# Performance work log

Hardware: AMD Instinct MI355X
Metric: run time of the kernel (lower is better)

## Reference

```python
import jax, jax.numpy as jnp
import numpy as np

B, N, M, C = 4, 4096, 300, 1152
SA_H, SA_D = 36, 32           # linear self-attention heads / head dim
CA_H = 16                     # cross-attention heads
INNER_SA = SA_H * SA_D        # 1152
INNER_FF = int(C * 2.5)       # 2880
EPS = 1e-6


def _ln(x):
    # LayerNorm without affine, eps=1e-6
    mu = x.mean(-1, keepdims=True)
    var = x.var(-1, keepdims=True)
    return (x - mu) / jnp.sqrt(var + EPS)


def setup_inputs() -> dict:
    key = jax.random.key(0)
    ks = jax.random.split(key, 24)
    p = lambda i, shape: jax.random.normal(ks[i], shape, jnp.float32) * 0.02
    return {
        "x": jax.random.normal(ks[0], (B, N, C), jnp.float32),
        "conditioning": jax.random.normal(ks[1], (B, M, C), jnp.float32),
        "t_emb": jax.random.normal(ks[2], (B, C), jnp.float32),
        # linear self-attention (qkv has no bias)
        "w_qkv": p(3, (C, 3 * INNER_SA)),
        "w_sa_out": p(4, (INNER_SA, C)),
        "b_sa_out": jnp.zeros((C,), jnp.float32),
        # norm_cross (affine LayerNorm)
        "gamma_cross": jnp.ones((C,), jnp.float32),
        "beta_cross": jnp.zeros((C,), jnp.float32),
        # cross-attention
        "w_q": p(5, (C, C)), "b_q": jnp.zeros((C,), jnp.float32),
        "w_kv": p(6, (C, 2 * C)), "b_kv": jnp.zeros((2 * C,), jnp.float32),
        "w_co": p(7, (C, C)), "b_co": jnp.zeros((C,), jnp.float32),
        # MixFFN
        "w_fc1": p(8, (C, 2 * INNER_FF)), "b_fc1": jnp.zeros((2 * INNER_FF,), jnp.float32),
        "dw_kernel": p(9, (3, 3, 1, INNER_FF)),  # depthwise conv, HWIO
        "dw_bias": jnp.zeros((INNER_FF,), jnp.float32),
        "w_fc2": p(10, (INNER_FF, C)), "b_fc2": jnp.zeros((C,), jnp.float32),
        # adaLN modulation
        "w_ada": p(11, (C, 6 * C)), "b_ada": jnp.zeros((6 * C,), jnp.float32),
        "sst": jax.random.normal(ks[12], (6, C), jnp.float32) * 0.02,
    }


def reference(x, conditioning, t_emb, w_qkv, w_sa_out, b_sa_out,
              gamma_cross, beta_cross, w_q, b_q, w_kv, b_kv, w_co, b_co,
              w_fc1, b_fc1, dw_kernel, dw_bias, w_fc2, b_fc2,
              w_ada, b_ada, sst):
    Bx, Nx, Cx = x.shape
    ada = jax.nn.silu(t_emb) @ w_ada + b_ada          # (B, 6C)
    ada = sst[None] + ada.reshape(Bx, 6, Cx)          # (B, 6, C)
    shift_sa, scale_sa, gate_sa, shift_ff, scale_ff, gate_ff = (
        ada[:, 0], ada[:, 1], ada[:, 2], ada[:, 3], ada[:, 4], ada[:, 5])

    # --- modulated linear self-attention (ReLU kernel) ---
    xn = _ln(x) * (1.0 + scale_sa[:, None]) + shift_sa[:, None]
    qkv = (xn @ w_qkv).reshape(Bx, Nx, 3, SA_H, SA_D)
    q = jax.nn.relu(qkv[:, :, 0])
    k = jax.nn.relu(qkv[:, :, 1])
    v = qkv[:, :, 2]
    kv = jnp.einsum('bnhd,bnhe->bhde', k, v)                  # (B,H,D,D)
    out = jnp.einsum('bnhd,bhde->bnhe', q, kv)                # (B,N,H,D)
    denom = jnp.einsum('bnhd,bhd->bnh', q, k.sum(1)) + 1e-6   # (B,N,H)
    out = (out / denom[..., None]).reshape(Bx, Nx, INNER_SA)
    x = x + gate_sa[:, None] * (out @ w_sa_out + b_sa_out)

    # --- cross-attention (softmax) ---
    xc = _ln(x) * gamma_cross + beta_cross
    hd = Cx // CA_H
    qc = (xc @ w_q + b_q).reshape(Bx, Nx, CA_H, hd)
    kvc = (conditioning @ w_kv + b_kv).reshape(Bx, M, 2, CA_H, hd)
    kc, vc = kvc[:, :, 0], kvc[:, :, 1]
    attn = jnp.einsum('bnhd,bmhd->bhnm', qc, kc) * (hd ** -0.5)
    attn = jax.nn.softmax(attn, axis=-1)
    oc = jnp.einsum('bhnm,bmhd->bnhd', attn, vc).reshape(Bx, Nx, Cx)
    x = x + oc @ w_co + b_co

    # --- modulated GLU-dwconv FFN ---
    xn = _ln(x) * (1.0 + scale_ff[:, None]) + shift_ff[:, None]
    gv = xn @ w_fc1 + b_fc1
    gate, val = gv[..., :INNER_FF], gv[..., INNER_FF:]
    h = jax.nn.silu(gate) * val
    hw = int(round(Nx ** 0.5))
    h = h.reshape(Bx, hw, hw, INNER_FF)                       # NHWC
    h = jax.lax.conv_general_dilated(
        h, dw_kernel, window_strides=(1, 1), padding='SAME',
        dimension_numbers=('NHWC', 'HWIO', 'NHWC'),
        feature_group_count=INNER_FF) + dw_bias
    h = h.reshape(Bx, Nx, INNER_FF)
    x = x + gate_ff[:, None] * (h @ w_fc2 + b_fc2)
    return x
```

## Files before the change

### kernel.cpp

```cpp
#include <hip/hip_runtime.h>

typedef __bf16 bf16_t;
typedef __attribute__((ext_vector_type(8))) __bf16 bf16x8;
typedef __attribute__((ext_vector_type(4))) __bf16 bf16x4;
typedef __attribute__((ext_vector_type(4))) float f32x4;

#define DEVINL __device__ __forceinline__

DEVINL void gload16(const void* g, void* l) {
  __builtin_amdgcn_global_load_lds(
      (const __attribute__((address_space(1))) void*)g,
      (__attribute__((address_space(3))) void*)l, 16, 0, 0);
}

template <int OUT>
__global__ __launch_bounds__(512) void gemm256r(
    const bf16_t* __restrict__ A, const bf16_t* __restrict__ Bt,
    void* __restrict__ Cv, int M, int N, int K,
    const float* __restrict__ bias, const float* __restrict__ resid,
    const float* __restrict__ gate, int GM)
{
  __shared__ __align__(16) bf16_t sL[2][2][256 * 32];
  const int tid = threadIdx.x;
  const int lane = tid & 63;
  const int wave = tid >> 6;
  const int wr = wave >> 2;
  const int wc = wave & 3;

  const int nbx = gridDim.x, nby = gridDim.y;
  const int nwg = nbx * nby;
  int lin = (int)blockIdx.y * nbx + (int)blockIdx.x;
  {
    const int q = nwg >> 3, rr = nwg & 7;
    const int xcd = lin & 7, idx = lin >> 3;
    lin = (xcd < rr ? xcd * (q + 1) : rr * (q + 1) + (xcd - rr) * q) + idx;
  }
  const int per_grp = GM * nbx;
  const int gid = lin / per_grp;
  const int rem = lin - gid * per_grp;
  const int gsz = min(GM, nby - gid * GM);
  const long tileM = (long)(gid * GM + rem % gsz) * 256;
  const long tileN = (long)(rem / gsz) * 256;

  const int r0 = tid >> 2;
  const int c0 = (((tid & 3) - (r0 >> 2)) & 3) * 8;

  auto STAGE = [&](int slot, int kt) {
    const bf16_t* ga = A + (tileM + r0) * (long)K + kt + c0;
    const bf16_t* gb = Bt + (tileN + r0) * (long)K + kt + c0;
    char* la = (char*)&sL[slot][0][0] + tid * 16;
    char* lb = (char*)&sL[slot][1][0] + tid * 16;
    gload16(ga, la);
    gload16(ga + 128 * (long)K, la + 8192);
    gload16(gb, lb);
    gload16(gb + 128 * (long)K, lb + 8192);
  };

  f32x4 acc[8][4] = {};
  const int NT = K >> 5;

  STAGE(0, 0); STAGE(1, 32);
  asm volatile("s_waitcnt vmcnt(4)" ::: "memory");
  asm volatile("s_barrier" ::: "memory");

  const int r = lane & 15;
  const int kg = lane >> 4;
  const int sw = ((kg + (r >> 2)) & 3) * 16;
  const int abyte = (wr * 128 + r) * 64 + sw;
  const int bbyte = (wc * 64 + r) * 64 + sw;

  for (int t = 0; t < NT; ++t) {
    const char* pA = (const char*)&sL[t & 1][0][0];
    const char* pB = (const char*)&sL[t & 1][1][0];
    bf16x8 a[8], b[4];
#pragma unroll
    for (int n = 0; n < 4; ++n) b[n] = *(const bf16x8*)(pB + bbyte + n * 1024);
#pragma unroll
    for (int m = 0; m < 8; ++m) a[m] = *(const bf16x8*)(pA + abyte + m * 1024);
    __builtin_amdgcn_s_setprio(1);
#pragma unroll
    for (int m = 0; m < 8; ++m)
#pragma unroll
      for (int n = 0; n < 4; ++n)
        acc[m][n] = __builtin_amdgcn_mfma_f32_16x16x32_bf16(a[m], b[n],
                                                            acc[m][n], 0, 0, 0);
    __builtin_amdgcn_s_setprio(0);
    if (t + 1 >= NT) break;
    asm volatile("s_waitcnt vmcnt(0)" ::: "memory");
    asm volatile("s_barrier" ::: "memory");
    if (t + 2 < NT) STAGE(t & 1, (t + 2) << 5);
  }

  const long row0 = tileM + wr * 128 + ((lane >> 4) * 4);
  const int col0 = (int)tileN + wc * 64 + r;
#pragma unroll
  for (int m = 0; m < 8; ++m) {
#pragma unroll
    for (int n = 0; n < 4; ++n) {
      const int col = col0 + n * 16;
      if (col < N) {
        const float bb = bias ? bias[col] : 0.0f;
#pragma unroll
        for (int j = 0; j < 4; ++j) {
          const long row = row0 + m * 16 + j;
          const long idx = row * (long)N + col;
          const float v = acc[m][n][j] + bb;
          if constexpr (OUT == 1) {
            const float g = gate ? gate[(row >> 12) * 6912 + col] : 1.0f;
            const float rv = resid ? resid[idx] : 0.0f;
            ((float*)Cv)[idx] = rv + g * v;
          } else {
            ((bf16_t*)Cv)[idx] = (bf16_t)v;
          }
        }
      }
    }
  }
}

template <int OUT>
__global__ __launch_bounds__(256) void gemm_bt(
    const bf16_t* __restrict__ A, const bf16_t* __restrict__ Bt,
    void* __restrict__ Cv, int M, int N, int K,
    long strideA, long strideB, long strideC,
    const float* __restrict__ bias, const float* __restrict__ resid,
    const float* __restrict__ gate, int GM)
{
  __shared__ __align__(16) bf16_t sA[128 * 32];
  __shared__ __align__(16) bf16_t sB[128 * 32];
  const int tid = threadIdx.x;
  const int lane = tid & 63;
  const int wave = tid >> 6;
  const bf16_t* Ab = A + (size_t)blockIdx.z * strideA;
  const bf16_t* Bb = Bt + (size_t)blockIdx.z * strideB;

  const int nbx = gridDim.x, nby = gridDim.y;
  const int nwg = nbx * nby;
  int lin = (int)blockIdx.y * nbx + (int)blockIdx.x;
  {
    const int q = nwg >> 3, rr = nwg & 7;
    const int xcd = lin & 7, idx = lin >> 3;
    lin = (xcd < rr ? xcd * (q + 1) : rr * (q + 1) + (xcd - rr) * q) + idx;
  }
  const int per_grp = GM * nbx;
  const int gid = lin / per_grp;
  const int rem = lin - gid * per_grp;
  const int gsz = min(GM, nby - gid * GM);
  const long tileM = (long)(gid * GM + rem % gsz) * 128;
  const long tileN = (long)(rem / gsz) * 128;
  const int wr = wave >> 1, wc = wave & 1;

  f32x4 acc[4][4] = {};

  const int srow = lane >> 2;
  const int skcol = (lane & 3) * 8;
  const bf16_t* gA0 = Ab + (tileM + wave * 16 + srow) * (long)K + skcol;
  const bf16_t* gB0 = Bb + (tileN + wave * 16 + srow) * (long)K + skcol;
  bf16_t* lA0 = sA + wave * 512;
  bf16_t* lB0 = sB + wave * 512;
  const long rs64 = 64L * K;

  const int aoff = (wr * 64 + (lane & 15)) * 32 + (lane >> 4) * 8;
  const int boff = (wc * 64 + (lane & 15)) * 32 + (lane >> 4) * 8;

  for (int kt = 0; kt < K; kt += 32) {
    __syncthreads();
    gload16(gA0 + kt, lA0);
    gload16(gA0 + kt + rs64, lA0 + 2048);
    gload16(gB0 + kt, lB0);
    gload16(gB0 + kt + rs64, lB0 + 2048);
    __syncthreads();
    bf16x8 av[4], bv[4];
#pragma unroll
    for (int m = 0; m < 4; ++m) av[m] = *(const bf16x8*)&sA[aoff + m * 512];
#pragma unroll
    for (int n = 0; n < 4; ++n) bv[n] = *(const bf16x8*)&sB[boff + n * 512];
#pragma unroll
    for (int m = 0; m < 4; ++m)
#pragma unroll
      for (int n = 0; n < 4; ++n)
        acc[m][n] = __builtin_amdgcn_mfma_f32_16x16x32_bf16(av[m], bv[n],
                                                            acc[m][n], 0, 0, 0);
  }

  const long row0 = tileM + wr * 64 + ((lane >> 4) * 4);
  const int col0 = (int)tileN + wc * 64 + (lane & 15);
#pragma unroll
  for (int m = 0; m < 4; ++m) {
#pragma unroll
    for (int n = 0; n < 4; ++n) {
      const int col = col0 + n * 16;
      const float bb = (OUT != 2 && bias) ? bias[col] : 0.0f;
#pragma unroll
      for (int j = 0; j < 4; ++j) {
        const long row = row0 + m * 16 + j;
        const float v = acc[m][n][j] + bb;
        if constexpr (OUT == 1) {
          const long idx = row * (long)N + col;
          const float g = gate ? gate[(row >> 12) * 6912 + col] : 1.0f;
          const float rv = resid ? resid[idx] : 0.0f;
          ((float*)Cv)[idx] = rv + g * v;
        } else if constexpr (OUT == 2) {
          if (col < 72)
            ((bf16_t*)Cv)[(((long)(blockIdx.z >> 4)) * 4096 + row) * 1152 +
                          (long)(blockIdx.z & 15) * 72 + col] = (bf16_t)v;
        } else if constexpr (OUT == 3) {
          const int h = col / 72, d = col - h * 72;
          const long b = row >> 12, n4 = row & 4095;
          ((bf16_t*)Cv)[((b * 16 + h) * 4096 + n4) * 96 + d] =
              (bf16_t)(v * 0.11785113019775793f);
        } else {
          const long idx = row * (long)N + col;
          (((bf16_t*)Cv) + (size_t)blockIdx.z * strideC)[idx] = (bf16_t)v;
        }
      }
    }
  }
}

__global__ __launch_bounds__(256) void transpose_cast(
    const float* __restrict__ W, bf16_t* __restrict__ WT, int K, int N)
{
  __shared__ float tile[32][33];
  const int n0 = blockIdx.x * 32, k0 = blockIdx.y * 32;
  const int tx = threadIdx.x & 31, ty = threadIdx.x >> 5;
#pragma unroll
  for (int r = ty; r < 32; r += 8) tile[r][tx] = W[(size_t)(k0 + r) * N + n0 + tx];
  __syncthreads();
#pragma unroll
  for (int r = ty; r < 32; r += 8)
    WT[(size_t)(n0 + r) * K + k0 + tx] = (bf16_t)tile[tx][r];
}

__global__ __launch_bounds__(256) void ada_kernel(
    const float* __restrict__ t_emb, const float* __restrict__ w_ada,
    const float* __restrict__ b_ada, const float* __restrict__ sst,
    float* __restrict__ ada)
{
  __shared__ float st[4][1152];
  const int t = threadIdx.x;
  const int j = blockIdx.x * 256 + t;
  for (int i = t; i < 4 * 1152; i += 256) {
    const int b = i / 1152, cc = i % 1152;
    const float v = t_emb[b * 1152 + cc];
    st[b][cc] = v / (1.0f + __expf(-v));
  }
  __syncthreads();
  const int k0 = blockIdx.y * 144;
  float a0 = 0.f, a1 = 0.f, a2 = 0.f, a3 = 0.f;
  for (int k = k0; k < k0 + 144; ++k) {
    const float w = w_ada[(size_t)k * 6912 + j];
    a0 += st[0][k] * w; a1 += st[1][k] * w;
    a2 += st[2][k] * w; a3 += st[3][k] * w;
  }
  if (blockIdx.y == 0) {
    const float base = b_ada[j] + sst[j];
    a0 += base; a1 += base; a2 += base; a3 += base;
  }
  atomicAdd(&ada[0 * 6912 + j], a0);
  atomicAdd(&ada[1 * 6912 + j], a1);
  atomicAdd(&ada[2 * 6912 + j], a2);
  atomicAdd(&ada[3 * 6912 + j], a3);
}

__global__ __launch_bounds__(256) void ln_mod(
    const float* __restrict__ X, bf16_t* __restrict__ out,
    const float* __restrict__ adaB, int shiftIdx, int scaleIdx,
    const float* __restrict__ gamma, const float* __restrict__ beta)
{
  const int row = blockIdx.x;
  const float4* xr4 = (const float4*)(X + (size_t)row * 1152);
  float s = 0.f, s2 = 0.f;
  for (int i = threadIdx.x; i < 288; i += 256) {
    const float4 v = xr4[i];
    s += v.x + v.y + v.z + v.w;
    s2 += v.x * v.x + v.y * v.y + v.z * v.z + v.w * v.w;
  }
  const int lane = threadIdx.x & 63, wave = threadIdx.x >> 6;
#pragma unroll
  for (int o = 32; o; o >>= 1) { s += __shfl_down(s, o); s2 += __shfl_down(s2, o); }
  __shared__ float rs[4], rq[4];
  if (lane == 0) { rs[wave] = s; rq[wave] = s2; }
  __syncthreads();
  if (threadIdx.x == 0) {
    rs[0] = rs[0] + rs[1] + rs[2] + rs[3];
    rq[0] = rq[0] + rq[1] + rq[2] + rq[3];
  }
  __syncthreads();
  const float mu = rs[0] * (1.0f / 1152.0f);
  const float var = rq[0] * (1.0f / 1152.0f) - mu * mu;
  const float inv = rsqrtf(var + 1e-6f);
  const int b = row >> 12;
  const float4* shiftv = (const float4*)(adaB ? adaB + b * 6912 + shiftIdx * 1152 : beta);
  const float4* scalev = (const float4*)(adaB ? adaB + b * 6912 + scaleIdx * 1152 : gamma);
  const float add1 = adaB ? 1.0f : 0.0f;
  for (int i = threadIdx.x; i < 288; i += 256) {
    const float4 v = xr4[i];
    const float4 sc = scalev[i];
    const float4 sh = shiftv[i];
    bf16x4 o;
    o[0] = (bf16_t)((v.x - mu) * inv * (add1 + sc.x) + sh.x);
    o[1] = (bf16_t)((v.y - mu) * inv * (add1 + sc.y) + sh.y);
    o[2] = (bf16_t)((v.z - mu) * inv * (add1 + sc.z) + sh.z);
    o[3] = (bf16_t)((v.w - mu) * inv * (add1 + sc.w) + sh.w);
    *(bf16x4*)&out[(size_t)row * 1152 + i * 4] = o;
  }
}

__global__ void pad_cond_k(const float* __restrict__ cond, bf16_t* __restrict__ condp)
{
  const int idx = blockIdx.x * 256 + threadIdx.x;
  const int row = idx / 1152;
  condp[idx] = (row < 1200) ? (bf16_t)cond[idx] : (bf16_t)0.0f;
}

__global__ __launch_bounds__(256) void sa_kv_k(
    const bf16_t* __restrict__ qkv, float* __restrict__ kvb, float* __restrict__ ksumb)
{
  const int bh = blockIdx.x, b = bh / 36, h = bh % 36;
  __shared__ bf16_t sk[32][32], sv[32][32];
  const int t = threadIdx.x;
  const int nn = t >> 5, c = t & 31;
  const int srow = (t & 127) >> 2;
  const int sq4 = (t & 3) * 8;
  const int isV = t >> 7;
  float a0 = 0.f, a1 = 0.f, a2 = 0.f, a3 = 0.f, ks = 0.f;
  const size_t rowbase = (size_t)b * 4096 + (size_t)blockIdx.y * 256;
  const size_t colbase = 1152 + (size_t)isV * 1152 + h * 32 + sq4;
  for (int n0 = 0; n0 < 256; n0 += 32) {
    __syncthreads();
    const bf16x8 v8 = *(const bf16x8*)&qkv[(rowbase + n0 + srow) * 3456 + colbase];
    if (isV == 0) {
      bf16x8 r8;
#pragma unroll
      for (int j = 0; j < 8; ++j) r8[j] = (bf16_t)fmaxf((float)v8[j], 0.0f);
      *(bf16x8*)&sk[srow][sq4] = r8;
    } else {
      *(bf16x8*)&sv[srow][sq4] = v8;
    }
    __syncthreads();
#pragma unroll
    for (int q = 0; q < 32; ++q) {
      const float vv = (float)sv[q][c];
      a0 += (float)sk[q][nn] * vv;
      a1 += (float)sk[q][nn + 8] * vv;
      a2 += (float)sk[q][nn + 16] * vv;
      a3 += (float)sk[q][nn + 24] * vv;
    }
    if (t < 32) {
#pragma unroll
      for (int q = 0; q < 32; ++q) ks += (float)sk[q][t];
    }
  }
  float* kvp = kvb + (size_t)bh * 1024;
  atomicAdd(&kvp[(nn + 0) * 32 + c], a0);
  atomicAdd(&kvp[(nn + 8) * 32 + c], a1);
  atomicAdd(&kvp[(nn + 16) * 32 + c], a2);
  atomicAdd(&kvp[(nn + 24) * 32 + c], a3);
  if (t < 32) atomicAdd(&ksumb[bh * 32 + t], ks);
}

__global__ __launch_bounds__(256) void sa_out_k(
    const bf16_t* __restrict__ qkv, const float* __restrict__ kvb,
    const float* __restrict__ ksumb, bf16_t* __restrict__ so)
{
  const int row0 = blockIdx.x * 8;
  const int b = row0 >> 12;
  __shared__ float q[8][1152];
  __shared__ float denom[8][36];
  const int t = threadIdx.x;
  for (int i = t; i < 1152; i += 256) {
    const int r = i / 144, c0 = (i % 144) * 8;
    const bf16x8 v8 = *(const bf16x8*)&qkv[(size_t)(row0 + r) * 3456 + c0];
#pragma unroll
    for (int j = 0; j < 8; ++j) q[r][c0 + j] = fmaxf((float)v8[j], 0.0f);
  }
  __syncthreads();
  for (int i = t; i < 288; i += 256) {
    int r = i / 36, h = i % 36;
    const float* ksp = ksumb + (b * 36 + h) * 32;
    float dsum = 1e-6f;
#pragma unroll
    for (int d = 0; d < 32; ++d) dsum += q[r][h * 32 + d] * ksp[d];
    denom[r][h] = dsum;
  }
  __syncthreads();
  for (int j = t; j < 1152; j += 256) {
    const int h = j >> 5, e = j & 31;
    const float* kvp = kvb + ((size_t)(b * 36 + h)) * 1024 + e;
    float kreg[32];
#pragma unroll
    for (int d = 0; d < 32; ++d) kreg[d] = kvp[d * 32];
#pragma unroll
    for (int r = 0; r < 8; ++r) {
      float a = 0.f;
#pragma unroll
      for (int d = 0; d < 32; ++d) a += q[r][h * 32 + d] * kreg[d];
      so[(size_t)(row0 + r) * 1152 + j] = (bf16_t)(a / denom[r][h]);
    }
  }
}

__global__ void ca_qrepack(const bf16_t* __restrict__ qc, bf16_t* __restrict__ qcp, int b)
{
  const size_t idx = (size_t)blockIdx.x * 256 + threadIdx.x;
  const int d = (int)(idx % 96);
  const size_t r = idx / 96;
  const int n = (int)(r & 4095);
  const int h = (int)(r >> 12);
  float v = 0.f;
  if (d < 72) v = (float)qc[((size_t)(b * 4096 + n)) * 1152 + h * 72 + d] * 0.11785113019775793f;
  qcp[idx] = (bf16_t)v;
}

__global__ void ca_kcrepack(const bf16_t* __restrict__ kvc, bf16_t* __restrict__ kcp, int b)
{
  const size_t idx = (size_t)blockIdx.x * 256 + threadIdx.x;
  const int d = (int)(idx % 96);
  const size_t r = idx / 96;
  const int m = (int)(r % 384);
  const int h = (int)(r / 384);
  bf16_t v = (bf16_t)0.0f;
  if (d < 72 && m < 300) v = kvc[((size_t)(b * 300 + m)) * 2304 + h * 72 + d];
  kcp[idx] = v;
}

__global__ void ca_vtrepack(const bf16_t* __restrict__ kvc, bf16_t* __restrict__ vt, int b)
{
  const size_t idx = (size_t)blockIdx.x * 256 + threadIdx.x;
  const int m = (int)(idx % 384);
  const size_t r = idx / 384;
  const int d = (int)(r & 127);
  const int h = (int)(r >> 7);
  bf16_t v = (bf16_t)0.0f;
  if (d < 72 && m < 300) v = kvc[((size_t)(b * 300 + m)) * 2304 + 1152 + h * 72 + d];
  vt[idx] = v;
}

__global__ __launch_bounds__(256) void softmax_k(bf16_t* __restrict__ s)
{
  const int row = blockIdx.x * 4 + (threadIdx.x >> 6);
  const int lane = threadIdx.x & 63;
  bf16_t* sr = s + (size_t)row * 384;
  float v[5];
  float mx = -1e30f;
#pragma unroll
  for (int i = 0; i < 5; ++i) {
    const int m = lane + 64 * i;
    v[i] = (m < 300) ? (float)sr[m] : -1e30f;
    mx = fmaxf(mx, v[i]);
  }
#pragma unroll
  for (int o = 32; o; o >>= 1) mx = fmaxf(mx, __shfl_xor(mx, o));
  float sum = 0.f;
#pragma unroll
  for (int i = 0; i < 5; ++i) { v[i] = __expf(v[i] - mx); sum += v[i]; }
#pragma unroll
  for (int o = 32; o; o >>= 1) sum += __shfl_xor(sum, o);
  const float inv = 1.0f / sum;
#pragma unroll
  for (int i = 0; i < 5; ++i) {
    const int m = lane + 64 * i;
    if (m < 320) sr[m] = (bf16_t)(v[i] * inv);
  }
}

__global__ void glu_k(const bf16_t* __restrict__ gv, bf16_t* __restrict__ h)
{
  const size_t idx = (size_t)blockIdx.x * 256 + threadIdx.x;
  const size_t row = idx / 360;
  const int c0 = (int)(idx % 360) * 8;
  const bf16x8 g8 = *(const bf16x8*)&gv[row * 5760 + c0];
  const bf16x8 v8 = *(const bf16x8*)&gv[row * 5760 + 2880 + c0];
  bf16x8 o;
#pragma unroll
  for (int j = 0; j < 8; ++j) {
    const float g = (float)g8[j];
    const float sg = g / (1.0f + __expf(-g));
    o[j] = (bf16_t)(sg * (float)v8[j]);
  }
  *(bf16x8*)&h[row * 2880 + c0] = o;
}

__global__ __launch_bounds__(256) void dwconv_k(
    const bf16_t* __restrict__ h, const float* __restrict__ wk,
    const float* __restrict__ wb, bf16_t* __restrict__ hc)
{
  const size_t idx = (size_t)blockIdx.x * 256 + threadIdx.x;
  const int c8 = (int)(idx % 360);
  size_t p = idx / 360;
  const int x = (int)(p & 63);
  const int y = (int)(p >> 6);
  const int c0 = c8 * 8;
  float acc[8];
#pragma unroll
  for (int j = 0; j < 8; ++j) acc[j] = wb[c0 + j];
  for (int ky = -1; ky <= 1; ++ky) {
    const int yy = y + ky;
    if (yy < 0 || yy > 63) continue;
    for (int kx = -1; kx <= 1; ++kx) {
      const int xx = x + kx;
      if (xx < 0 || xx > 63) continue;
      const bf16x8 v = *(const bf16x8*)&h[((size_t)(yy * 64 + xx)) * 2880 + c0];
      const float* w = wk + ((ky + 1) * 3 + (kx + 1)) * 2880 + c0;
#pragma unroll
      for (int j = 0; j < 8; ++j) acc[j] += (float)v[j] * w[j];
    }
  }
  bf16x8 o;
#pragma unroll
  for (int j = 0; j < 8; ++j) o[j] = (bf16_t)acc[j];
  *(bf16x8*)&hc[((size_t)(y * 64 + x)) * 2880 + c0] = o;
}

extern "C" void kernel_launch(void* const* d_in, const int* in_sizes, int n_in,
                              void* d_out, int out_size, void* d_ws, size_t ws_size,
                              hipStream_t stream)
{
  const float* x          = (const float*)d_in[0];
  const float* cond       = (const float*)d_in[1];
  const float* t_emb      = (const float*)d_in[2];
  const float* w_qkv      = (const float*)d_in[3];
  const float* w_sa_out   = (const float*)d_in[4];
  const float* b_sa_out   = (const float*)d_in[5];
  const float* gamma_cr   = (const float*)d_in[6];
  const float* beta_cr    = (const float*)d_in[7];
  const float* w_q        = (const float*)d_in[8];
  const float* b_q        = (const float*)d_in[9];
  const float* w_kv       = (const float*)d_in[10];
  const float* b_kv       = (const float*)d_in[11];
  const float* w_co       = (const float*)d_in[12];
  const float* b_co       = (const float*)d_in[13];
  const float* w_fc1      = (const float*)d_in[14];
  const float* b_fc1      = (const float*)d_in[15];
  const float* dw_kernel  = (const float*)d_in[16];
  const float* dw_bias    = (const float*)d_in[17];
  const float* w_fc2      = (const float*)d_in[18];
  const float* b_fc2      = (const float*)d_in[19];
  const float* w_ada      = (const float*)d_in[20];
  const float* b_ada      = (const float*)d_in[21];
  const float* sst        = (const float*)d_in[22];
  float* out = (float*)d_out;

  char* ws = (char*)d_ws;
  size_t off = 0;
  auto alloc = [&](size_t bytes) -> char* {
    off = (off + 255) & ~(size_t)255;
    char* p = ws + off;
    off += bytes;
    return p;
  };

  bf16_t* wqkvT  = (bf16_t*)alloc((size_t)3584 * 1152 * 2);
  bf16_t* wsaT   = (bf16_t*)alloc((size_t)1280 * 1152 * 2);
  bf16_t* wqT    = (bf16_t*)alloc((size_t)1280 * 1152 * 2);
  bf16_t* wkvT   = (bf16_t*)alloc((size_t)2304 * 1152 * 2);
  bf16_t* wcoT   = (bf16_t*)alloc((size_t)1280 * 1152 * 2);
  bf16_t* wfc1T  = (bf16_t*)alloc((size_t)5888 * 1152 * 2);
  bf16_t* wfc2T  = (bf16_t*)alloc((size_t)1280 * 2880 * 2);
  float*  adaB   = (float*)alloc((size_t)4 * 6912 * 4);
  bf16_t* xn     = (bf16_t*)alloc((size_t)16384 * 1152 * 2);
  bf16_t* buf37  = (bf16_t*)alloc((size_t)16384 * 1152 * 2);
  float*  kvb    = (float*)alloc((size_t)144 * 1024 * 4);
  float*  ksumb  = (float*)alloc((size_t)144 * 32 * 4);
  bf16_t* condp  = (bf16_t*)alloc((size_t)1280 * 1152 * 2);
  bf16_t* kvcB   = (bf16_t*)alloc((size_t)1280 * 2304 * 2);

  const size_t ARENA_SMALL = (size_t)16384 * 3456 * 2;
  const size_t CA_Q = (size_t)64 * 4096 * 96 * 2;
  const size_t CA_K = (size_t)64 * 384 * 96 * 2;
  const size_t CA_V = (size_t)64 * 128 * 384 * 2;
  const size_t CA_S = (size_t)64 * 4096 * 384 * 2;
  const size_t ARENA_BIG = CA_Q + CA_K + CA_V + CA_S;
  const bool big = (off + 512 + ARENA_BIG) <= ws_size;
  char* arena = alloc(big ? ARENA_BIG : ARENA_SMALL);
  if (off > ws_size) return;

  bf16_t* qkvB = (bf16_t*)arena;
  bf16_t *qcp, *kcp, *vcT, *scores;
  if (big) {
    qcp    = (bf16_t*)arena;
    kcp    = (bf16_t*)(arena + CA_Q);
    vcT    = (bf16_t*)(arena + CA_Q + CA_K);
    scores = (bf16_t*)(arena + CA_Q + CA_K + CA_V);
  } else {
    qcp    = (bf16_t*)arena;
    kcp    = (bf16_t*)(arena + 12582912);
    vcT    = (bf16_t*)(arena + 12582912 + 1179648);
    scores = (bf16_t*)(arena + 12582912 + 1179648 + 1572864);
  }
  bf16_t *gvB, *hB, *hcB;
  if (big) {
    gvB = (bf16_t*)arena;
    hB  = (bf16_t*)(arena + (size_t)8192 * 5760 * 2);
    hcB = (bf16_t*)(arena + (size_t)8192 * 5760 * 2 + (size_t)8192 * 2880 * 2);
  } else {
    hcB = (bf16_t*)arena;
    gvB = (bf16_t*)(arena + (size_t)8192 * 2880 * 2);
    hB  = buf37;
  }

  hipMemsetAsync(adaB, 0, (size_t)4 * 6912 * 4, stream);
  hipMemsetAsync(kvb, 0, (size_t)144 * 1024 * 4, stream);
  hipMemsetAsync(ksumb, 0, (size_t)144 * 32 * 4, stream);

  transpose_cast<<<dim3(108, 36), 256, 0, stream>>>(w_qkv, wqkvT, 1152, 3456);
  transpose_cast<<<dim3(36, 36), 256, 0, stream>>>(w_sa_out, wsaT, 1152, 1152);
  transpose_cast<<<dim3(36, 36), 256, 0, stream>>>(w_q, wqT, 1152, 1152);
  transpose_cast<<<dim3(72, 36), 256, 0, stream>>>(w_kv, wkvT, 1152, 2304);
  transpose_cast<<<dim3(36, 36), 256, 0, stream>>>(w_co, wcoT, 1152, 1152);
  transpose_cast<<<dim3(180, 36), 256, 0, stream>>>(w_fc1, wfc1T, 1152, 5760);
  transpose_cast<<<dim3(36, 90), 256, 0, stream>>>(w_fc2, wfc2T, 2880, 1152);
  ada_kernel<<<dim3(27, 8), 256, 0, stream>>>(t_emb, w_ada, b_ada, sst, adaB);
  pad_cond_k<<<5760, 256, 0, stream>>>(cond, condp);

  ln_mod<<<16384, 256, 0, stream>>>(x, xn, adaB, 0, 1, nullptr, nullptr);
  gemm256r<0><<<dim3(14, 64), 512, 0, stream>>>(xn, wqkvT, qkvB, 16384, 3456, 1152,
                                                nullptr, nullptr, nullptr, 8);
  sa_kv_k<<<dim3(144, 16), 256, 0, stream>>>(qkvB, kvb, ksumb);
  sa_out_k<<<2048, 256, 0, stream>>>(qkvB, kvb, ksumb, buf37);
  gemm_bt<1><<<dim3(9, 128), 256, 0, stream>>>(buf37, wsaT, out, 16384, 1152, 1152,
                                               0, 0, 0, b_sa_out, x, adaB + 2 * 1152, 8);

  ln_mod<<<16384, 256, 0, stream>>>(out, xn, nullptr, 0, 0, gamma_cr, beta_cr);
  gemm_bt<0><<<dim3(18, 10, 1), 256, 0, stream>>>(condp, wkvT, kvcB, 1280, 2304, 1152,
                                                  0, 0, 0, b_kv, nullptr, nullptr, 8);
  if (big) {
    hipMemsetAsync(qcp, 0, CA_Q, stream);
    gemm_bt<3><<<dim3(9, 128), 256, 0, stream>>>(xn, wqT, qcp, 16384, 1152, 1152,
                                                 0, 0, 0, b_q, nullptr, nullptr, 8);
    for (int b = 0; b < 4; ++b) {
      ca_kcrepack<<<2304, 256, 0, stream>>>(kvcB, kcp + (size_t)b * 16 * 384 * 96, b);
      ca_vtrepack<<<3072, 256, 0, stream>>>(kvcB, vcT + (size_t)b * 16 * 128 * 384, b);
    }
    gemm_bt<0><<<dim3(3, 32, 64), 256, 0, stream>>>(qcp, kcp, scores, 4096, 384, 96,
                                                    (long)4096 * 96, (long)384 * 96,
                                                    (long)4096 * 384, nullptr, nullptr, nullptr, 8);
    softmax_k<<<65536, 256, 0, stream>>>(scores);
    gemm_bt<2><<<dim3(1, 32, 64), 256, 0, stream>>>(scores, vcT, buf37, 4096, 128, 384,
                                                    (long)4096 * 384, (long)128 * 384,
                                                    0, nullptr, nullptr, nullptr, 8);
  } else {
    gemm_bt<0><<<dim3(9, 128), 256, 0, stream>>>(xn, wqT, buf37, 16384, 1152, 1152,
                                                 0, 0, 0, b_q, nullptr, nullptr, 8);
    for (int b = 0; b < 4; ++b) {
      ca_qrepack<<<24576, 256, 0, stream>>>(buf37, qcp, b);
      ca_kcrepack<<<2304, 256, 0, stream>>>(kvcB, kcp, b);
      ca_vtrepack<<<3072, 256, 0, stream>>>(kvcB, vcT, b);
      gemm_bt<0><<<dim3(3, 32, 16), 256, 0, stream>>>(qcp, kcp, scores, 4096, 384, 96,
                                                      (long)4096 * 96, (long)384 * 96,
                                                      (long)4096 * 384, nullptr, nullptr, nullptr, 8);
      softmax_k<<<16384, 256, 0, stream>>>(scores);
      gemm_bt<2><<<dim3(1, 32, 16), 256, 0, stream>>>(scores, vcT,
                                                      buf37 + (size_t)b * 4096 * 1152,
                                                      4096, 128, 384,
                                                      (long)4096 * 384, (long)128 * 384,
                                                      0, nullptr, nullptr, nullptr, 8);
    }
  }
  gemm_bt<1><<<dim3(9, 128), 256, 0, stream>>>(buf37, wcoT, out, 16384, 1152, 1152,
                                               0, 0, 0, b_co, out, nullptr, 8);

  ln_mod<<<16384, 256, 0, stream>>>(out, xn, adaB, 3, 4, nullptr, nullptr);
  if (big) {
    for (int c = 0; c < 2; ++c) {
      gemm256r<0><<<dim3(23, 32), 512, 0, stream>>>(xn + (size_t)c * 8192 * 1152, wfc1T,
                                                    gvB, 8192, 5760, 1152,
                                                    b_fc1, nullptr, nullptr, 8);
      glu_k<<<11520, 256, 0, stream>>>(gvB, hB);
      for (int bb = 0; bb < 2; ++bb)
        dwconv_k<<<5760, 256, 0, stream>>>(hB + (size_t)bb * 4096 * 2880,
                                           dw_kernel, dw_bias,
                                           hcB + (size_t)(c * 2 + bb) * 4096 * 2880);
    }
    gemm_bt<1><<<dim3(9, 128), 256, 0, stream>>>(hcB, wfc2T, out, 16384, 1152, 2880,
                                                 0, 0, 0, b_fc2, out,
                                                 adaB + 5 * 1152, 8);
  } else {
    for (int c = 0; c < 2; ++c) {
      for (int bb = 0; bb < 2; ++bb) {
        const int b = c * 2 + bb;
        gemm256r<0><<<dim3(23, 16), 512, 0, stream>>>(xn + (size_t)b * 4096 * 1152, wfc1T,
                                                      gvB, 4096, 5760, 1152,
                                                      b_fc1, nullptr, nullptr, 8);
        glu_k<<<5760, 256, 0, stream>>>(gvB, hB);
        dwconv_k<<<5760, 256, 0, stream>>>(hB, dw_kernel, dw_bias,
                                           hcB + (size_t)bb * 4096 * 2880);
      }
      gemm_bt<1><<<dim3(9, 64), 256, 0, stream>>>(hcB, wfc2T,
                                                  out + (size_t)c * 8192 * 1152,
                                                  8192, 1152, 2880, 0, 0, 0, b_fc2,
                                                  out + (size_t)c * 8192 * 1152,
                                                  adaB + (size_t)c * 2 * 6912 + 5 * 1152, 8);
    }
  }

  (void)in_sizes; (void)n_in; (void)out_size; (void)ws_size;
}
```

Before: 1.891 ms.

## Fuse SiLU-GLU into fc1 GEMM epilogue and triple-buffer gemm256r LDS

The fc1 weight is repacked so that each 32-column block interleaves 16 gate columns with their 16 matching value columns. The gemm256r epilogue can then compute silu(gate)*value directly and write the 2880-wide hidden tensor, which removes the separate glu kernel and the round trip of the 5760-wide intermediate through memory. The GEMM main loop also moves from double to triple buffering in LDS, with the waitcnt adjusted so two tiles stay in flight. In exchange, LDS use rises to 96KB per block, which may lower occupancy, and the epilogue now writes scalar bf16 values rather than vectors.

Result: faster. 1.784 ms (-5.7%).

```diff
diff --git a/kernel.cpp b/kernel.cpp
--- a/kernel.cpp
+++ b/kernel.cpp
@@ -20,7 +20,7 @@
     const float* __restrict__ bias, const float* __restrict__ resid,
     const float* __restrict__ gate, int GM)
 {
-  __shared__ __align__(16) bf16_t sL[2][2][256 * 32];
+  __shared__ __align__(16) bf16_t sL[3][2][256 * 32];
   const int tid = threadIdx.x;
   const int lane = tid & 63;
   const int wave = tid >> 6;
@@ -59,8 +59,8 @@
   f32x4 acc[8][4] = {};
   const int NT = K >> 5;
 
-  STAGE(0, 0); STAGE(1, 32);
-  asm volatile("s_waitcnt vmcnt(4)" ::: "memory");
+  STAGE(0, 0); STAGE(1, 32); STAGE(2, 64);
+  asm volatile("s_waitcnt vmcnt(8)" ::: "memory");
   asm volatile("s_barrier" ::: "memory");
 
   const int r = lane & 15;
@@ -69,9 +69,10 @@
   const int abyte = (wr * 128 + r) * 64 + sw;
   const int bbyte = (wc * 64 + r) * 64 + sw;
 
+  int slot = 0;
   for (int t = 0; t < NT; ++t) {
-    const char* pA = (const char*)&sL[t & 1][0][0];
-    const char* pB = (const char*)&sL[t & 1][1][0];
+    const char* pA = (const char*)&sL[slot][0][0];
+    const char* pB = (const char*)&sL[slot][1][0];
     bf16x8 a[8], b[4];
 #pragma unroll
     for (int n = 0; n < 4; ++n) b[n] = *(const bf16x8*)(pB + bbyte + n * 1024);
@@ -86,13 +87,38 @@
                                                             acc[m][n], 0, 0, 0);
     __builtin_amdgcn_s_setprio(0);
     if (t + 1 >= NT) break;
-    asm volatile("s_waitcnt vmcnt(0)" ::: "memory");
+    if (t + 2 < NT) asm volatile("s_waitcnt vmcnt(4)" ::: "memory");
+    else            asm volatile("s_waitcnt vmcnt(0)" ::: "memory");
     asm volatile("s_barrier" ::: "memory");
-    if (t + 2 < NT) STAGE(t & 1, (t + 2) << 5);
+    if (t + 3 < NT) STAGE(slot, (t + 3) << 5);
+    slot = (slot == 2) ? 0 : slot + 1;
   }
 
   const long row0 = tileM + wr * 128 + ((lane >> 4) * 4);
   const int col0 = (int)tileN + wc * 64 + r;
+  if constexpr (OUT == 4) {
+#pragma unroll
+    for (int m = 0; m < 8; ++m) {
+#pragma unroll
+      for (int n = 0; n < 4; n += 2) {
+        const int base = (int)tileN + wc * 64 + n * 16;
+        if (base < 5760) {
+          const int hcol = (base >> 1) + r;
+          const float bg = bias[hcol];
+          const float bv = bias[2880 + hcol];
+#pragma unroll
+          for (int j = 0; j < 4; ++j) {
+            const long row = row0 + m * 16 + j;
+            const float g = acc[m][n][j] + bg;
+            const float v = acc[m][n + 1][j] + bv;
+            const float sg = g / (1.0f + __expf(-g));
+            ((bf16_t*)Cv)[row * 2880 + hcol] = (bf16_t)(sg * v);
+          }
+        }
+      }
+    }
+    return;
+  }
 #pragma unroll
   for (int m = 0; m < 8; ++m) {
 #pragma unroll
@@ -232,6 +258,26 @@
     WT[(size_t)(n0 + r) * K + k0 + tx] = (bf16_t)tile[tx][r];
 }
 
+__global__ __launch_bounds__(256) void transpose_glu(
+    const float* __restrict__ W, bf16_t* __restrict__ WT)
+{
+  __shared__ float tile[32][33];
+  const int b = blockIdx.x;
+  const int k0 = blockIdx.y * 32;
+  const int tx = threadIdx.x & 31, ty = threadIdx.x >> 5;
+  if (b < 180) {
+    const int src = (tx < 16) ? (b * 16 + tx) : (2880 + b * 16 + tx - 16);
+#pragma unroll
+    for (int r = ty; r < 32; r += 8)
+      tile[r][tx] = W[(size_t)(k0 + r) * 5760 + src];
+  }
+  __syncthreads();
+#pragma unroll
+  for (int o = ty; o < 32; o += 8)
+    WT[(size_t)(b * 32 + o) * 1152 + k0 + tx] =
+        (b < 180) ? (bf16_t)tile[tx][o] : (bf16_t)0.0f;
+}
+
 __global__ __launch_bounds__(256) void ada_kernel(
     const float* __restrict__ t_emb, const float* __restrict__ w_ada,
     const float* __restrict__ b_ada, const float* __restrict__ sst,
@@ -463,23 +509,6 @@
     const int m = lane + 64 * i;
     if (m < 320) sr[m] = (bf16_t)(v[i] * inv);
   }
-}
-
-__global__ void glu_k(const bf16_t* __restrict__ gv, bf16_t* __restrict__ h)
-{
-  const size_t idx = (size_t)blockIdx.x * 256 + threadIdx.x;
-  const size_t row = idx / 360;
-  const int c0 = (int)(idx % 360) * 8;
-  const bf16x8 g8 = *(const bf16x8*)&gv[row * 5760 + c0];
-  const bf16x8 v8 = *(const bf16x8*)&gv[row * 5760 + 2880 + c0];
-  bf16x8 o;
-#pragma unroll
-  for (int j = 0; j < 8; ++j) {
-    const float g = (float)g8[j];
-    const float sg = g / (1.0f + __expf(-g));
-    o[j] = (bf16_t)(sg * (float)v8[j]);
-  }
-  *(bf16x8*)&h[row * 2880 + c0] = o;
 }
 
 __global__ __launch_bounds__(256) void dwconv_k(
@@ -556,7 +585,7 @@
   bf16_t* wqT    = (bf16_t*)alloc((size_t)1280 * 1152 * 2);
   bf16_t* wkvT   = (bf16_t*)alloc((size_t)2304 * 1152 * 2);
   bf16_t* wcoT   = (bf16_t*)alloc((size_t)1280 * 1152 * 2);
-  bf16_t* wfc1T  = (bf16_t*)alloc((size_t)5888 * 1152 * 2);
+  bf16_t* wfc1P  = (bf16_t*)alloc((size_t)5888 * 1152 * 2);
   bf16_t* wfc2T  = (bf16_t*)alloc((size_t)1280 * 2880 * 2);
   float*  adaB   = (float*)alloc((size_t)4 * 6912 * 4);
   bf16_t* xn     = (bf16_t*)alloc((size_t)16384 * 1152 * 2);
@@ -589,14 +618,12 @@
     vcT    = (bf16_t*)(arena + 12582912 + 1179648);
     scores = (bf16_t*)(arena + 12582912 + 1179648 + 1572864);
   }
-  bf16_t *gvB, *hB, *hcB;
+  bf16_t *hB, *hcB;
   if (big) {
-    gvB = (bf16_t*)arena;
-    hB  = (bf16_t*)(arena + (size_t)8192 * 5760 * 2);
-    hcB = (bf16_t*)(arena + (size_t)8192 * 5760 * 2 + (size_t)8192 * 2880 * 2);
+    hB  = (bf16_t*)arena;
+    hcB = (bf16_t*)(arena + (size_t)8192 * 2880 * 2);
   } else {
     hcB = (bf16_t*)arena;
-    gvB = (bf16_t*)(arena + (size_t)8192 * 2880 * 2);
     hB  = buf37;
   }
 
@@ -609,7 +636,7 @@
   transpose_cast<<<dim3(36, 36), 256, 0, stream>>>(w_q, wqT, 1152, 1152);
   transpose_cast<<<dim3(72, 36), 256, 0, stream>>>(w_kv, wkvT, 1152, 2304);
   transpose_cast<<<dim3(36, 36), 256, 0, stream>>>(w_co, wcoT, 1152, 1152);
-  transpose_cast<<<dim3(180, 36), 256, 0, stream>>>(w_fc1, wfc1T, 1152, 5760);
+  transpose_glu<<<dim3(184, 36), 256, 0, stream>>>(w_fc1, wfc1P);
   transpose_cast<<<dim3(36, 90), 256, 0, stream>>>(w_fc2, wfc2T, 2880, 1152);
   ada_kernel<<<dim3(27, 8), 256, 0, stream>>>(t_emb, w_ada, b_ada, sst, adaB);
   pad_cond_k<<<5760, 256, 0, stream>>>(cond, condp);
@@ -664,10 +691,9 @@
   ln_mod<<<16384, 256, 0, stream>>>(out, xn, adaB, 3, 4, nullptr, nullptr);
   if (big) {
     for (int c = 0; c < 2; ++c) {
-      gemm256r<0><<<dim3(23, 32), 512, 0, stream>>>(xn + (size_t)c * 8192 * 1152, wfc1T,
-                                                    gvB, 8192, 5760, 1152,
+      gemm256r<4><<<dim3(23, 32), 512, 0, stream>>>(xn + (size_t)c * 8192 * 1152, wfc1P,
+                                                    hB, 8192, 5760, 1152,
                                                     b_fc1, nullptr, nullptr, 8);
-      glu_k<<<11520, 256, 0, stream>>>(gvB, hB);
       for (int bb = 0; bb < 2; ++bb)
         dwconv_k<<<5760, 256, 0, stream>>>(hB + (size_t)bb * 4096 * 2880,
                                            dw_kernel, dw_bias,
@@ -680,10 +706,9 @@
     for (int c = 0; c < 2; ++c) {
       for (int bb = 0; bb < 2; ++bb) {
         const int b = c * 2 + bb;
-        gemm256r<0><<<dim3(23, 16), 512, 0, stream>>>(xn + (size_t)b * 4096 * 1152, wfc1T,
-                                                      gvB, 4096, 5760, 1152,
+        gemm256r<4><<<dim3(23, 16), 512, 0, stream>>>(xn + (size_t)b * 4096 * 1152, wfc1P,
+                                                      hB, 4096, 5760, 1152,
                                                       b_fc1, nullptr, nullptr, 8);
-        glu_k<<<5760, 256, 0, stream>>>(gvB, hB);
         dwconv_k<<<5760, 256, 0, stream>>>(hB, dw_kernel, dw_bias,
                                            hcB + (size_t)bb * 4096 * 2880);
       }
```
